# Performance work log

Measured on AMD Instinct MI355X. Metric: run time of the kernel, lower is better.

## Reference

```python
import jax, jax.numpy as jnp
import numpy as np

N, E, F_IN, H, C = 100000, 1600000, 128, 128, 40

def setup_inputs() -> dict:
    key = jax.random.key(0)
    ks = jax.random.split(key, 8)
    s = 0.05  # param init scale
    return {
        "x": jax.random.normal(ks[0], (N, F_IN), dtype=jnp.float32),
        "edge_index": jax.random.randint(ks[1], (2, E), 0, N, dtype=jnp.int64),
        "W1_rel": jax.random.normal(ks[2], (H, F_IN), dtype=jnp.float32) * s,
        "b1": jnp.zeros((H,), dtype=jnp.float32),
        "W1_root": jax.random.normal(ks[3], (H, F_IN), dtype=jnp.float32) * s,
        "W2_rel": jax.random.normal(ks[4], (C, H), dtype=jnp.float32) * s,
        "b2": jnp.zeros((C,), dtype=jnp.float32),
        "W2_root": jax.random.normal(ks[5], (C, H), dtype=jnp.float32) * s,
    }

def _graph_conv(x, src, dst, W_rel, b, W_root, n_nodes):
    # PyG GraphConv: lin_rel(sum_{j in N(i)} x_j) + lin_root(x_i); lin_root has no bias
    agg = jax.ops.segment_sum(x[src], dst, num_segments=n_nodes)  # [N, F]
    return agg @ W_rel.T + b + x @ W_root.T

def reference(x, edge_index, W1_rel, b1, W1_root, W2_rel, b2, W2_root):
    src, dst = edge_index[0], edge_index[1]
    h = _graph_conv(x, src, dst, W1_rel, b1, W1_root, N)
    h = jax.nn.relu(h)  # dropout is identity in eval mode
    out = _graph_conv(h, src, dst, W2_rel, b2, W2_root, N)
    return jax.nn.log_softmax(out, axis=1)
```

## Files before the change

kernel.cpp:

```cpp
#include <hip/hip_runtime.h>
#include <hip/hip_bf16.h>
#include <math.h>

typedef __bf16 bf16x8 __attribute__((ext_vector_type(8)));
typedef float f32x4 __attribute__((ext_vector_type(4)));
typedef float f32x2 __attribute__((ext_vector_type(2)));
typedef unsigned int uint32;

#define CHUNK 4096
#define MAXBINS 512

__device__ __forceinline__ float bflo(uint32 u) { return __uint_as_float(u << 16); }
__device__ __forceinline__ float bfhi(uint32 u) { return __uint_as_float(u & 0xffff0000u); }
__device__ __forceinline__ unsigned short tobf(float f) {
    return __builtin_bit_cast(unsigned short, __float2bfloat16(f));
}
__device__ __forceinline__ unsigned char tofp8(float f) {
    return (unsigned char)(__builtin_amdgcn_cvt_pk_fp8_f32(f, f, 0, false) & 0xff);
}


__global__ __launch_bounds__(256) void binhist_kernel(
    const int* __restrict__ dst, int* __restrict__ blkhist,
    int nE, int nChunks, int nBins)
{
    __shared__ int h[MAXBINS];
    int blk = blockIdx.x, t = threadIdx.x;
    for (int i = t; i < nBins; i += 256) h[i] = 0;
    __syncthreads();
    int e0 = blk * CHUNK;
    int e1 = e0 + CHUNK; if (e1 > nE) e1 = nE;
    for (int e = e0 + t; e < e1; e += 256)
        atomicAdd(&h[dst[e] >> 8], 1);
    __syncthreads();
    for (int b = t; b < nBins; b += 256)
        blkhist[(size_t)b * nChunks + blk] = h[b];
}

__global__ __launch_bounds__(256) void csr_partial_kernel(
    const int* __restrict__ cnt, int* __restrict__ blocksum, int nN)
{
    int b = blockIdx.x, t = threadIdx.x;
    int base = b * 1024 + t * 4;
    int s = 0;
    #pragma unroll
    for (int k = 0; k < 4; ++k) { int i = base + k; if (i < nN) s += cnt[i]; }
    #pragma unroll
    for (int off = 1; off < 64; off <<= 1) s += __shfl_xor(s, off);
    __shared__ int ws[4];
    int lane = t & 63, w = t >> 6;
    if (lane == 0) ws[w] = s;
    __syncthreads();
    if (t == 0) blocksum[b] = ws[0] + ws[1] + ws[2] + ws[3];
}

__global__ __launch_bounds__(1024) void csr_scanblocks_kernel(
    const int* __restrict__ blocksum, int* __restrict__ blockpre,
    int nB, int* __restrict__ outtot, int nN)
{
    __shared__ int sm[1024];
    int t = threadIdx.x;
    int v = (t < nB) ? blocksum[t] : 0;
    sm[t] = v;
    __syncthreads();
    for (int off = 1; off < 1024; off <<= 1) {
        int u = (t >= off) ? sm[t - off] : 0;
        __syncthreads();
        sm[t] += u;
        __syncthreads();
    }
    if (t < nB) blockpre[t] = sm[t] - v;
    if (t == 1023) outtot[nN] = sm[1023];
}

__global__ __launch_bounds__(256) void csr_scanfinal_kernel(
    const int* __restrict__ cnt, const int* __restrict__ blockpre,
    int* __restrict__ out, int nN)
{
    int b = blockIdx.x, t = threadIdx.x;
    int base = b * 1024 + t * 4;
    int c[4]; int s = 0;
    #pragma unroll
    for (int k = 0; k < 4; ++k) { int i = base + k; c[k] = (i < nN) ? cnt[i] : 0; s += c[k]; }
    int lane = t & 63, w = t >> 6;
    int inc = s;
    #pragma unroll
    for (int off = 1; off < 64; off <<= 1) {
        int u = __shfl_up(inc, off);
        if (lane >= off) inc += u;
    }
    __shared__ int ws[4];
    if (lane == 63) ws[w] = inc;
    __syncthreads();
    int wpre = 0;
    for (int i = 0; i < w; ++i) wpre += ws[i];
    int run = blockpre[b] + wpre + (inc - s);
    #pragma unroll
    for (int k = 0; k < 4; ++k) {
        int i = base + k;
        if (i < nN) { out[i] = run; run += c[k]; }
    }
}

__global__ __launch_bounds__(256) void binscatter_kernel(
    const int* __restrict__ src, const int* __restrict__ dst,
    const int* __restrict__ blkbase, uint32* __restrict__ packed,
    int nE, int nChunks, int nBins)
{
    __shared__ int h[MAXBINS];
    int blk = blockIdx.x, t = threadIdx.x;
    for (int i = t; i < nBins; i += 256) h[i] = 0;
    __syncthreads();
    int e0 = blk * CHUNK;
    int e1 = e0 + CHUNK; if (e1 > nE) e1 = nE;
    for (int e = e0 + t; e < e1; e += 256) {
        int d = dst[e];
        int b = d >> 8;
        int r = atomicAdd(&h[b], 1);
        int pos = blkbase[(size_t)b * nChunks + blk] + r;
        packed[pos] = (uint32)src[e] | ((uint32)(d & 255) << 24);
    }
}

__global__ __launch_bounds__(256) void binsort_kernel(
    const uint32* __restrict__ packed, const int* __restrict__ blkbase,
    int* __restrict__ rowptr, int* __restrict__ sorted_src,
    int nChunks, int nBins, int nN, int nE)
{
    __shared__ int h[256];
    __shared__ int offs[256];
    __shared__ int ws[4];
    int b = blockIdx.x, t = threadIdx.x;
    int segbase = blkbase[(size_t)b * nChunks];
    int segend  = (b + 1 < nBins) ? blkbase[(size_t)(b + 1) * nChunks] : nE;

    h[t] = 0;
    __syncthreads();
    for (int i = segbase + t; i < segend; i += 256)
        atomicAdd(&h[packed[i] >> 24], 1);
    __syncthreads();

    int c = h[t];
    int lane = t & 63, w = t >> 6;
    int inc = c;
    #pragma unroll
    for (int off = 1; off < 64; off <<= 1) {
        int u = __shfl_up(inc, off);
        if (lane >= off) inc += u;
    }
    if (lane == 63) ws[w] = inc;
    __syncthreads();
    int wpre = 0;
    for (int i = 0; i < w; ++i) wpre += ws[i];
    int ex = wpre + inc - c;
    offs[t] = ex;
    int node = b * 256 + t;
    if (node < nN) rowptr[node] = segbase + ex;
    if (b == 0 && t == 0) rowptr[nN] = nE;
    __syncthreads();

    for (int i = segbase + t; i < segend; i += 256) {
        uint32 pk = packed[i];
        int ld = (int)(pk >> 24);
        int r = atomicAdd(&offs[ld], 1);
        sorted_src[segbase + r] = (int)(pk & 0x00FFFFFFu);
    }
}

__global__ __launch_bounds__(256) void prep_all_kernel(
    const float4* __restrict__ xin, uint32* __restrict__ xf8out, int n4,
    const float* __restrict__ W1_rel, const float* __restrict__ W1_root,
    const float* __restrict__ W2_rel, const float* __restrict__ W2_root,
    unsigned short* __restrict__ W1relB, unsigned short* __restrict__ W1rootB,
    unsigned short* __restrict__ Wpq)
{
    if (blockIdx.x < 168) {
        int i = blockIdx.x * 256 + threadIdx.x;
        if (i < 16384) {
            W1relB[i] = tobf(W1_rel[i]);
        } else if (i < 32768) {
            int j = i - 16384;
            W1rootB[j] = tobf(W1_root[j]);
        } else if (i < 32768 + 10240) {
            int j = i - 32768;
            int o = j >> 7, k = j & 127;
            float v = (o < 40) ? W2_rel[o * 128 + k] : W2_root[(o - 40) * 128 + k];
            Wpq[j] = tobf(v);
        }
    } else {
        int i = (blockIdx.x - 168) * 256 + threadIdx.x;
        int stride = (gridDim.x - 168) * 256;
        for (; i < n4; i += stride) {
            float4 v = xin[i];
            int w = __builtin_amdgcn_cvt_pk_fp8_f32(v.x, v.y, 0, false);
            w = __builtin_amdgcn_cvt_pk_fp8_f32(v.z, v.w, w, true);
            xf8out[i] = (uint32)w;
        }
    }
}

__global__ __launch_bounds__(256) void aggregate_fp8_kernel(
    const uint32* __restrict__ xf8u,
    const int* __restrict__ rowptr,
    const int* __restrict__ sorted_src,
    uint2* __restrict__ aggout2,
    int nN)
{
    int wave = threadIdx.x >> 6;
    int lane = threadIdx.x & 63;
    int node = blockIdx.x * 4 + wave;
    if (node >= nN) return;
    int half = lane >> 5, l32 = lane & 31;
    int beg = rowptr[node], end = rowptr[node + 1];
    float a0 = 0.f, a1 = 0.f, a2 = 0.f, a3 = 0.f;
    int j = beg;
    for (; j + 16 <= end; j += 16) {
        uint32 u0 = xf8u[(size_t)sorted_src[j + half] * 32 + l32];
        uint32 u1 = xf8u[(size_t)sorted_src[j + 2 + half] * 32 + l32];
        uint32 u2 = xf8u[(size_t)sorted_src[j + 4 + half] * 32 + l32];
        uint32 u3 = xf8u[(size_t)sorted_src[j + 6 + half] * 32 + l32];
        uint32 u4 = xf8u[(size_t)sorted_src[j + 8 + half] * 32 + l32];
        uint32 u5 = xf8u[(size_t)sorted_src[j + 10 + half] * 32 + l32];
        uint32 u6 = xf8u[(size_t)sorted_src[j + 12 + half] * 32 + l32];
        uint32 u7 = xf8u[(size_t)sorted_src[j + 14 + half] * 32 + l32];
        f32x2 p0 = __builtin_amdgcn_cvt_pk_f32_fp8(u0, false);
        f32x2 q0 = __builtin_amdgcn_cvt_pk_f32_fp8(u0, true);
        f32x2 p1 = __builtin_amdgcn_cvt_pk_f32_fp8(u1, false);
        f32x2 q1 = __builtin_amdgcn_cvt_pk_f32_fp8(u1, true);
        f32x2 p2 = __builtin_amdgcn_cvt_pk_f32_fp8(u2, false);
        f32x2 q2 = __builtin_amdgcn_cvt_pk_f32_fp8(u2, true);
        f32x2 p3 = __builtin_amdgcn_cvt_pk_f32_fp8(u3, false);
        f32x2 q3 = __builtin_amdgcn_cvt_pk_f32_fp8(u3, true);
        f32x2 p4 = __builtin_amdgcn_cvt_pk_f32_fp8(u4, false);
        f32x2 q4 = __builtin_amdgcn_cvt_pk_f32_fp8(u4, true);
        f32x2 p5 = __builtin_amdgcn_cvt_pk_f32_fp8(u5, false);
        f32x2 q5 = __builtin_amdgcn_cvt_pk_f32_fp8(u5, true);
        f32x2 p6 = __builtin_amdgcn_cvt_pk_f32_fp8(u6, false);
        f32x2 q6 = __builtin_amdgcn_cvt_pk_f32_fp8(u6, true);
        f32x2 p7 = __builtin_amdgcn_cvt_pk_f32_fp8(u7, false);
        f32x2 q7 = __builtin_amdgcn_cvt_pk_f32_fp8(u7, true);
        a0 += ((p0[0] + p1[0]) + (p2[0] + p3[0])) + ((p4[0] + p5[0]) + (p6[0] + p7[0]));
        a1 += ((p0[1] + p1[1]) + (p2[1] + p3[1])) + ((p4[1] + p5[1]) + (p6[1] + p7[1]));
        a2 += ((q0[0] + q1[0]) + (q2[0] + q3[0])) + ((q4[0] + q5[0]) + (q6[0] + q7[0]));
        a3 += ((q0[1] + q1[1]) + (q2[1] + q3[1])) + ((q4[1] + q5[1]) + (q6[1] + q7[1]));
    }
    for (; j + 8 <= end; j += 8) {
        uint32 u0 = xf8u[(size_t)sorted_src[j + half] * 32 + l32];
        uint32 u1 = xf8u[(size_t)sorted_src[j + 2 + half] * 32 + l32];
        uint32 u2 = xf8u[(size_t)sorted_src[j + 4 + half] * 32 + l32];
        uint32 u3 = xf8u[(size_t)sorted_src[j + 6 + half] * 32 + l32];
        f32x2 p0 = __builtin_amdgcn_cvt_pk_f32_fp8(u0, false);
        f32x2 q0 = __builtin_amdgcn_cvt_pk_f32_fp8(u0, true);
        f32x2 p1 = __builtin_amdgcn_cvt_pk_f32_fp8(u1, false);
        f32x2 q1 = __builtin_amdgcn_cvt_pk_f32_fp8(u1, true);
        f32x2 p2 = __builtin_amdgcn_cvt_pk_f32_fp8(u2, false);
        f32x2 q2 = __builtin_amdgcn_cvt_pk_f32_fp8(u2, true);
        f32x2 p3 = __builtin_amdgcn_cvt_pk_f32_fp8(u3, false);
        f32x2 q3 = __builtin_amdgcn_cvt_pk_f32_fp8(u3, true);
        a0 += (p0[0] + p1[0]) + (p2[0] + p3[0]);
        a1 += (p0[1] + p1[1]) + (p2[1] + p3[1]);
        a2 += (q0[0] + q1[0]) + (q2[0] + q3[0]);
        a3 += (q0[1] + q1[1]) + (q2[1] + q3[1]);
    }
    for (; j + 2 <= end; j += 2) {
        uint32 u = xf8u[(size_t)sorted_src[j + half] * 32 + l32];
        f32x2 p0 = __builtin_amdgcn_cvt_pk_f32_fp8(u, false);
        f32x2 p1 = __builtin_amdgcn_cvt_pk_f32_fp8(u, true);
        a0 += p0[0]; a1 += p0[1]; a2 += p1[0]; a3 += p1[1];
    }
    if (j < end && half == 0) {
        uint32 u = xf8u[(size_t)sorted_src[j] * 32 + l32];
        f32x2 p0 = __builtin_amdgcn_cvt_pk_f32_fp8(u, false);
        f32x2 p1 = __builtin_amdgcn_cvt_pk_f32_fp8(u, true);
        a0 += p0[0]; a1 += p0[1]; a2 += p1[0]; a3 += p1[1];
    }
    a0 += __shfl_xor(a0, 32);
    a1 += __shfl_xor(a1, 32);
    a2 += __shfl_xor(a2, 32);
    a3 += __shfl_xor(a3, 32);
    if (half == 0) {
        uint2 o;
        o.x = (uint32)tobf(a0) | ((uint32)tobf(a1) << 16);
        o.y = (uint32)tobf(a2) | ((uint32)tobf(a3) << 16);
        aggout2[(size_t)node * 32 + l32] = o;
    }
}

__global__ __launch_bounds__(256) void gemm_fused_kernel(
    const unsigned short* __restrict__ aggb,
    const float* __restrict__ xf,
    const unsigned short* __restrict__ Wrel,
    const unsigned short* __restrict__ Wroot,
    const unsigned short* __restrict__ Wpq,
    const float* __restrict__ b1,
    unsigned char* __restrict__ pf8,
    unsigned short* __restrict__ qb,
    int nN)
{
    __shared__ __align__(16) unsigned char lds[32768];
    __shared__ __align__(16) unsigned char hlds[16384];
    int tid = threadIdx.x;
    int wave = tid >> 6, lane = tid & 63;
    int i0 = blockIdx.x * 64 + wave * 16;
    int mrow = lane & 15, kslot = lane >> 4;
    int arow = i0 + mrow; if (arow >= nN) arow = 0;

    f32x4 acc[8] = {};
    const unsigned short* Wsrc[2] = {Wrel, Wroot};

    for (int ph = 0; ph < 2; ++ph) {
        __syncthreads();
        const uint4* src = (const uint4*)Wsrc[ph];
        for (int c = tid; c < 2048; c += 256) {
            int row = c >> 4;
            int off = (c & 15) << 4;
            *(uint4*)(&lds[row * 256 + (off ^ ((row & 7) << 4))]) = src[c];
        }
        __syncthreads();
        if (ph == 0) {
            const unsigned short* Ap = aggb + (size_t)arow * 128 + kslot * 8;
            #pragma unroll
            for (int t = 0; t < 4; ++t) {
                bf16x8 a = *(const bf16x8*)(Ap + t * 32);
                #pragma unroll
                for (int ct = 0; ct < 8; ++ct) {
                    int o = ct * 16 + mrow;
                    int off = (t * 64 + kslot * 16) ^ ((o & 7) << 4);
                    bf16x8 b = *(const bf16x8*)(&lds[o * 256 + off]);
                    acc[ct] = __builtin_amdgcn_mfma_f32_16x16x32_bf16(a, b, acc[ct], 0, 0, 0);
                }
            }
        } else {
            const float* Ap = xf + (size_t)arow * 128 + kslot * 8;
            #pragma unroll
            for (int t = 0; t < 4; ++t) {
                float4 f0 = *(const float4*)(Ap + t * 32);
                float4 f1 = *(const float4*)(Ap + t * 32 + 4);
                union { bf16x8 v; unsigned short u[8]; } a;
                a.u[0] = tobf(f0.x); a.u[1] = tobf(f0.y);
                a.u[2] = tobf(f0.z); a.u[3] = tobf(f0.w);
                a.u[4] = tobf(f1.x); a.u[5] = tobf(f1.y);
                a.u[6] = tobf(f1.z); a.u[7] = tobf(f1.w);
                #pragma unroll
                for (int ct = 0; ct < 8; ++ct) {
                    int o = ct * 16 + mrow;
                    int off = (t * 64 + kslot * 16) ^ ((o & 7) << 4);
                    bf16x8 b = *(const bf16x8*)(&lds[o * 256 + off]);
                    acc[ct] = __builtin_amdgcn_mfma_f32_16x16x32_bf16(a.v, b, acc[ct], 0, 0, 0);
                }
            }
        }
    }

    #pragma unroll
    for (int ct = 0; ct < 8; ++ct) {
        int col = ct * 16 + mrow;
        float bias = b1[col];
        #pragma unroll
        for (int r = 0; r < 4; ++r) {
            int rl = wave * 16 + kslot * 4 + r;
            float v = fmaxf(acc[ct][r] + bias, 0.f);
            *(unsigned short*)(&hlds[rl * 256 + ((col * 2) ^ ((rl & 7) << 4))]) = tobf(v);
        }
    }
    __syncthreads();

    {
        const uint4* src = (const uint4*)Wpq;
        for (int c = tid; c < 1280; c += 256) {
            int row = c >> 4;
            int off = (c & 15) << 4;
            *(uint4*)(&lds[row * 256 + (off ^ ((row & 7) << 4))]) = src[c];
        }
    }
    __syncthreads();

    f32x4 acc2[5] = {};
    {
        int rl = wave * 16 + mrow;
        #pragma unroll
        for (int t = 0; t < 4; ++t) {
            bf16x8 a = *(const bf16x8*)(&hlds[rl * 256 + ((t * 64 + kslot * 16) ^ ((rl & 7) << 4))]);
            #pragma unroll
            for (int ct = 0; ct < 5; ++ct) {
                int o = ct * 16 + mrow;
                int off = (t * 64 + kslot * 16) ^ ((o & 7) << 4);
                bf16x8 b = *(const bf16x8*)(&lds[o * 256 + off]);
                acc2[ct] = __builtin_amdgcn_mfma_f32_16x16x32_bf16(a, b, acc2[ct], 0, 0, 0);
            }
        }
    }

    #pragma unroll
    for (int ct = 0; ct < 5; ++ct) {
        int col = ct * 16 + mrow;
        #pragma unroll
        for (int r = 0; r < 4; ++r) {
            int row = i0 + kslot * 4 + r;
            if (row < nN) {
                if (col < 40) pf8[(size_t)row * 64 + col] = tofp8(acc2[ct][r]);
                else          qb[(size_t)row * 40 + (col - 40)] = tobf(acc2[ct][r]);
            }
        }
    }
}

__global__ __launch_bounds__(256) void final_lsm_kernel(
    const unsigned short* __restrict__ pf8u,
    const uint32* __restrict__ qbu,
    const int* __restrict__ rowptr,
    const int* __restrict__ sorted_src,
    const float* __restrict__ b2,
    float* __restrict__ out,
    int nN)
{
    int wave = threadIdx.x >> 6;
    int lane = threadIdx.x & 63;
    int node = blockIdx.x * 4 + wave;
    if (node >= nN) return;

    int esub = (lane >= 40) ? 2 : (lane >= 20 ? 1 : 0);
    int cp   = lane - esub * 20;
    bool active = lane < 60;
    int beg = rowptr[node], end = rowptr[node + 1];

    float a0 = 0.f, a1 = 0.f;
    int j = beg;
    if (active) {
        for (; j + 9 <= end; j += 9) {
            int s0 = sorted_src[j + esub];
            int s1 = sorted_src[j + 3 + esub];
            int s2 = sorted_src[j + 6 + esub];
            uint32 u0 = pf8u[(size_t)s0 * 32 + cp];
            uint32 u1 = pf8u[(size_t)s1 * 32 + cp];
            uint32 u2 = pf8u[(size_t)s2 * 32 + cp];
            f32x2 p0 = __builtin_amdgcn_cvt_pk_f32_fp8(u0, false);
            f32x2 p1 = __builtin_amdgcn_cvt_pk_f32_fp8(u1, false);
            f32x2 p2 = __builtin_amdgcn_cvt_pk_f32_fp8(u2, false);
            a0 += (p0[0] + p1[0]) + p2[0];
            a1 += (p0[1] + p1[1]) + p2[1];
        }
        for (; j + 3 <= end; j += 3) {
            uint32 u = pf8u[(size_t)sorted_src[j + esub] * 32 + cp];
            f32x2 p = __builtin_amdgcn_cvt_pk_f32_fp8(u, false);
            a0 += p[0]; a1 += p[1];
        }
        int rem = end - j;
        if (esub < rem) {
            uint32 u = pf8u[(size_t)sorted_src[j + esub] * 32 + cp];
            f32x2 p = __builtin_amdgcn_cvt_pk_f32_fp8(u, false);
            a0 += p[0]; a1 += p[1];
        }
    }
    {
        float t0 = __shfl(a0, cp + 20), t1 = __shfl(a0, cp + 40);
        float t2 = __shfl(a1, cp + 20), t3 = __shfl(a1, cp + 40);
        a0 += t0 + t1;
        a1 += t2 + t3;
    }

    float v0, v1;
    if (lane < 20) {
        uint32 uq = qbu[(size_t)node * 20 + lane];
        float2 bb = *(const float2*)(b2 + 2 * lane);
        v0 = a0 + bflo(uq) + bb.x;
        v1 = a1 + bfhi(uq) + bb.y;
    } else {
        v0 = v1 = -INFINITY;
    }

    float m = fmaxf(v0, v1);
    #pragma unroll
    for (int off = 32; off >= 1; off >>= 1) m = fmaxf(m, __shfl_xor(m, off));
    float s = (lane < 20) ? (expf(v0 - m) + expf(v1 - m)) : 0.f;
    #pragma unroll
    for (int off = 32; off >= 1; off >>= 1) s += __shfl_xor(s, off);
    float lse = m + logf(s);

    if (lane < 20) {
        float2 o = make_float2(v0 - lse, v1 - lse);
        *(float2*)(out + (size_t)node * 40 + 2 * lane) = o;
    }
}


static inline char* alignup(char* p, size_t a) {
    return (char*)(((uintptr_t)p + a - 1) & ~(uintptr_t)(a - 1));
}

extern "C" void kernel_launch(void* const* d_in, const int* in_sizes, int n_in,
                              void* d_out, int out_size, void* d_ws, size_t ws_size,
                              hipStream_t stream)
{
    const float* x       = (const float*)d_in[0];
    const int*   ei      = (const int*)d_in[1];
    const float* W1_rel  = (const float*)d_in[2];
    const float* b1      = (const float*)d_in[3];
    const float* W1_root = (const float*)d_in[4];
    const float* W2_rel  = (const float*)d_in[5];
    const float* b2      = (const float*)d_in[6];
    const float* W2_root = (const float*)d_in[7];

    int N = in_sizes[0] / 128;
    int E = in_sizes[1] / 2;
    const int* srcp = ei;
    const int* dstp = ei + E;

    int nChunks = (E + CHUNK - 1) / CHUNK;
    int nBins   = (N + 255) >> 8;
    int nScan   = nBins * nChunks;
    int nB2     = (nScan + 1023) / 1024;
    size_t nf = (size_t)N * 128;

    char* p = (char*)d_ws;
    unsigned char*  xf8     = (unsigned char*)p;   p += nf;
    unsigned short* aggb    = (unsigned short*)p;  p += nf * 2;
    p = alignup(p, 64);
    unsigned char*  pf8     = (unsigned char*)p;   p += (size_t)N * 64;
    p = alignup(p, 16);
    unsigned short* qb      = (unsigned short*)p;  p += (size_t)N * 40 * 2;
    p = alignup(p, 16);
    unsigned short* W1relB  = (unsigned short*)p;  p += 16384 * 2;
    unsigned short* W1rootB = (unsigned short*)p;  p += 16384 * 2;
    unsigned short* Wpq     = (unsigned short*)p;  p += 10240 * 2;
    p = alignup(p, 16);
    int* rowptr     = (int*)p;  p += (size_t)(N + 1) * 4;
    p = alignup(p, 16);
    int* blkhist    = (int*)p;  p += (size_t)nScan * 4;
    int* blkbase    = (int*)p;  p += (size_t)(nScan + 1) * 4;
    int* blocksum   = (int*)p;  p += (size_t)nB2 * 4;
    int* blockpre   = (int*)p;  p += (size_t)nB2 * 4;
    p = alignup(p, 16);
    uint32* packed  = (uint32*)p; p += (size_t)E * 4;
    p = alignup(p, 16);
    int* sorted_src = (int*)p;  p += (size_t)E * 4;

    if ((size_t)(p - (char*)d_ws) > ws_size || nBins > MAXBINS) return;

    binhist_kernel<<<nChunks, 256, 0, stream>>>(dstp, blkhist, E, nChunks, nBins);
    csr_partial_kernel<<<nB2, 256, 0, stream>>>(blkhist, blocksum, nScan);
    csr_scanblocks_kernel<<<1, 1024, 0, stream>>>(blocksum, blockpre, nB2, blkbase, nScan);
    csr_scanfinal_kernel<<<nB2, 256, 0, stream>>>(blkhist, blockpre, blkbase, nScan);
    binscatter_kernel<<<nChunks, 256, 0, stream>>>(srcp, dstp, blkbase, packed, E, nChunks, nBins);
    binsort_kernel<<<nBins, 256, 0, stream>>>(packed, blkbase, rowptr, sorted_src,
                                              nChunks, nBins, N, E);

    prep_all_kernel<<<168 + 2048, 256, 0, stream>>>(
        (const float4*)x, (uint32*)xf8, (int)(nf / 4),
        W1_rel, W1_root, W2_rel, W2_root, W1relB, W1rootB, Wpq);

    aggregate_fp8_kernel<<<(N + 3) / 4, 256, 0, stream>>>(
        (const uint32*)xf8, rowptr, sorted_src, (uint2*)aggb, N);

    gemm_fused_kernel<<<(N + 63) / 64, 256, 0, stream>>>(
        aggb, x, W1relB, W1rootB, Wpq, b1, pf8, qb, N);

    final_lsm_kernel<<<(N + 3) / 4, 256, 0, stream>>>(
        (const unsigned short*)pf8, (const uint32*)qb, rowptr, sorted_src,
        b2, (float*)d_out, N);
}
```

Measured before the change: 196.1 us.

## Pack fp8 layer-2 features densely and predicate gather tails

```diff
diff --git a/kernel.cpp b/kernel.cpp
--- a/kernel.cpp
+++ b/kernel.cpp
@@ -244,35 +244,19 @@
         a2 += ((q0[0] + q1[0]) + (q2[0] + q3[0])) + ((q4[0] + q5[0]) + (q6[0] + q7[0]));
         a3 += ((q0[1] + q1[1]) + (q2[1] + q3[1])) + ((q4[1] + q5[1]) + (q6[1] + q7[1]));
     }
-    for (; j + 8 <= end; j += 8) {
-        uint32 u0 = xf8u[(size_t)sorted_src[j + half] * 32 + l32];
-        uint32 u1 = xf8u[(size_t)sorted_src[j + 2 + half] * 32 + l32];
-        uint32 u2 = xf8u[(size_t)sorted_src[j + 4 + half] * 32 + l32];
-        uint32 u3 = xf8u[(size_t)sorted_src[j + 6 + half] * 32 + l32];
-        f32x2 p0 = __builtin_amdgcn_cvt_pk_f32_fp8(u0, false);
-        f32x2 q0 = __builtin_amdgcn_cvt_pk_f32_fp8(u0, true);
-        f32x2 p1 = __builtin_amdgcn_cvt_pk_f32_fp8(u1, false);
-        f32x2 q1 = __builtin_amdgcn_cvt_pk_f32_fp8(u1, true);
-        f32x2 p2 = __builtin_amdgcn_cvt_pk_f32_fp8(u2, false);
-        f32x2 q2 = __builtin_amdgcn_cvt_pk_f32_fp8(u2, true);
-        f32x2 p3 = __builtin_amdgcn_cvt_pk_f32_fp8(u3, false);
-        f32x2 q3 = __builtin_amdgcn_cvt_pk_f32_fp8(u3, true);
-        a0 += (p0[0] + p1[0]) + (p2[0] + p3[0]);
-        a1 += (p0[1] + p1[1]) + (p2[1] + p3[1]);
-        a2 += (q0[0] + q1[0]) + (q2[0] + q3[0]);
-        a3 += (q0[1] + q1[1]) + (q2[1] + q3[1]);
-    }
-    for (; j + 2 <= end; j += 2) {
-        uint32 u = xf8u[(size_t)sorted_src[j + half] * 32 + l32];
-        f32x2 p0 = __builtin_amdgcn_cvt_pk_f32_fp8(u, false);
-        f32x2 p1 = __builtin_amdgcn_cvt_pk_f32_fp8(u, true);
-        a0 += p0[0]; a1 += p0[1]; a2 += p1[0]; a3 += p1[1];
-    }
-    if (j < end && half == 0) {
-        uint32 u = xf8u[(size_t)sorted_src[j] * 32 + l32];
-        f32x2 p0 = __builtin_amdgcn_cvt_pk_f32_fp8(u, false);
-        f32x2 p1 = __builtin_amdgcn_cvt_pk_f32_fp8(u, true);
-        a0 += p0[0]; a1 += p0[1]; a2 += p1[0]; a3 += p1[1];
+    {
+        uint32 u[8] = {0, 0, 0, 0, 0, 0, 0, 0};
+        #pragma unroll
+        for (int k = 0; k < 8; ++k) {
+            int e = j + 2 * k + half;
+            if (e < end) u[k] = xf8u[(size_t)sorted_src[e] * 32 + l32];
+        }
+        #pragma unroll
+        for (int k = 0; k < 8; ++k) {
+            f32x2 p = __builtin_amdgcn_cvt_pk_f32_fp8(u[k], false);
+            f32x2 q = __builtin_amdgcn_cvt_pk_f32_fp8(u[k], true);
+            a0 += p[0]; a1 += p[1]; a2 += q[0]; a3 += q[1];
+        }
     }
     a0 += __shfl_xor(a0, 32);
     a1 += __shfl_xor(a1, 32);
@@ -398,7 +382,7 @@
         for (int r = 0; r < 4; ++r) {
             int row = i0 + kslot * 4 + r;
             if (row < nN) {
-                if (col < 40) pf8[(size_t)row * 64 + col] = tofp8(acc2[ct][r]);
+                if (col < 40) pf8[(size_t)row * 40 + col] = tofp8(acc2[ct][r]);
                 else          qb[(size_t)row * 40 + (col - 40)] = tobf(acc2[ct][r]);
             }
         }
@@ -424,6 +408,13 @@
     bool active = lane < 60;
     int beg = rowptr[node], end = rowptr[node + 1];
 
+    uint32 uq = 0;
+    float2 bb = make_float2(0.f, 0.f);
+    if (lane < 20) {
+        uq = qbu[(size_t)node * 20 + lane];
+        bb = *(const float2*)(b2 + 2 * lane);
+    }
+
     float a0 = 0.f, a1 = 0.f;
     int j = beg;
     if (active) {
@@ -431,26 +422,25 @@
             int s0 = sorted_src[j + esub];
             int s1 = sorted_src[j + 3 + esub];
             int s2 = sorted_src[j + 6 + esub];
-            uint32 u0 = pf8u[(size_t)s0 * 32 + cp];
-            uint32 u1 = pf8u[(size_t)s1 * 32 + cp];
-            uint32 u2 = pf8u[(size_t)s2 * 32 + cp];
+            uint32 u0 = pf8u[(size_t)s0 * 20 + cp];
+            uint32 u1 = pf8u[(size_t)s1 * 20 + cp];
+            uint32 u2 = pf8u[(size_t)s2 * 20 + cp];
             f32x2 p0 = __builtin_amdgcn_cvt_pk_f32_fp8(u0, false);
             f32x2 p1 = __builtin_amdgcn_cvt_pk_f32_fp8(u1, false);
             f32x2 p2 = __builtin_amdgcn_cvt_pk_f32_fp8(u2, false);
             a0 += (p0[0] + p1[0]) + p2[0];
             a1 += (p0[1] + p1[1]) + p2[1];
         }
-        for (; j + 3 <= end; j += 3) {
-            uint32 u = pf8u[(size_t)sorted_src[j + esub] * 32 + cp];
-            f32x2 p = __builtin_amdgcn_cvt_pk_f32_fp8(u, false);
-            a0 += p[0]; a1 += p[1];
-        }
-        int rem = end - j;
-        if (esub < rem) {
-            uint32 u = pf8u[(size_t)sorted_src[j + esub] * 32 + cp];
-            f32x2 p = __builtin_amdgcn_cvt_pk_f32_fp8(u, false);
-            a0 += p[0]; a1 += p[1];
-        }
+        int e0 = j + esub, e1 = j + 3 + esub, e2 = j + 6 + esub;
+        uint32 u0 = 0, u1 = 0, u2 = 0;
+        if (e0 < end) u0 = pf8u[(size_t)sorted_src[e0] * 20 + cp];
+        if (e1 < end) u1 = pf8u[(size_t)sorted_src[e1] * 20 + cp];
+        if (e2 < end) u2 = pf8u[(size_t)sorted_src[e2] * 20 + cp];
+        f32x2 p0 = __builtin_amdgcn_cvt_pk_f32_fp8(u0, false);
+        f32x2 p1 = __builtin_amdgcn_cvt_pk_f32_fp8(u1, false);
+        f32x2 p2 = __builtin_amdgcn_cvt_pk_f32_fp8(u2, false);
+        a0 += (p0[0] + p1[0]) + p2[0];
+        a1 += (p0[1] + p1[1]) + p2[1];
     }
     {
         float t0 = __shfl(a0, cp + 20), t1 = __shfl(a0, cp + 40);
@@ -461,8 +451,6 @@
 
     float v0, v1;
     if (lane < 20) {
-        uint32 uq = qbu[(size_t)node * 20 + lane];
-        float2 bb = *(const float2*)(b2 + 2 * lane);
         v0 = a0 + bflo(uq) + bb.x;
         v1 = a1 + bfhi(uq) + bb.y;
     } else {
@@ -471,10 +459,10 @@
 
     float m = fmaxf(v0, v1);
     #pragma unroll
-    for (int off = 32; off >= 1; off >>= 1) m = fmaxf(m, __shfl_xor(m, off));
+    for (int off = 16; off >= 1; off >>= 1) m = fmaxf(m, __shfl_xor(m, off));
     float s = (lane < 20) ? (expf(v0 - m) + expf(v1 - m)) : 0.f;
     #pragma unroll
-    for (int off = 32; off >= 1; off >>= 1) s += __shfl_xor(s, off);
+    for (int off = 16; off >= 1; off >>= 1) s += __shfl_xor(s, off);
     float lse = m + logf(s);
 
     if (lane < 20) {
@@ -515,8 +503,8 @@
     char* p = (char*)d_ws;
     unsigned char*  xf8     = (unsigned char*)p;   p += nf;
     unsigned short* aggb    = (unsigned short*)p;  p += nf * 2;
-    p = alignup(p, 64);
-    unsigned char*  pf8     = (unsigned char*)p;   p += (size_t)N * 64;
+    p = alignup(p, 16);
+    unsigned char*  pf8     = (unsigned char*)p;   p += (size_t)N * 40 + 64;
     p = alignup(p, 16);
     unsigned short* qb      = (unsigned short*)p;  p += (size_t)N * 40 * 2;
     p = alignup(p, 16);
```

New measurement: 187.4 us, median of 2. 4.4% less time.
